# Kernel optimization log

Hardware: AMD Instinct MI355X
Metric: run time of the kernel (lower is better)

The kernel has to match this reference:

```python
import jax, jax.numpy as jnp
from jax import lax
import numpy as np

EPS = 1e-6
B, CIN, HW = 16, 12, 40
E, DEPTH, NH = 768, 12, 12
K, PAD = 10, 5
S = (HW + 2 * PAD - K) // 1 + 1  # 41 (series_len = s0); s1 also 41
L = S * S
HD = E // NH
MLP = 4 * E


def _ln(x, w, b):
    mu = x.mean(-1, keepdims=True)
    xc = x - mu
    var = (xc * xc).mean(-1, keepdims=True)
    return xc * lax.rsqrt(var + EPS) * w + b


def setup_inputs() -> dict:
    key = jax.random.key(0)
    ks = iter(jax.random.split(key, 24))
    r = lambda shape, s=0.02: jax.random.normal(next(ks), shape, jnp.float32) * s
    inp = {
        'x': jax.random.normal(next(ks), (B, CIN, HW, HW), jnp.float32),
        'conv_w': r((E, CIN, K, K)), 'conv_b': jnp.zeros((E,), jnp.float32),
        'pos_embed': r((1, L, E)),
        'ln1_w': jnp.ones((DEPTH, E), jnp.float32), 'ln1_b': jnp.zeros((DEPTH, E), jnp.float32),
        'qkv_w': r((DEPTH, E, 3 * E)), 'qkv_b': jnp.zeros((DEPTH, 3 * E), jnp.float32),
        'proj_w': r((DEPTH, E, E)), 'proj_b': jnp.zeros((DEPTH, E), jnp.float32),
        'ln2_w': jnp.ones((DEPTH, E), jnp.float32), 'ln2_b': jnp.zeros((DEPTH, E), jnp.float32),
        'fc1_w': r((DEPTH, E, MLP)), 'fc1_b': jnp.zeros((DEPTH, MLP), jnp.float32),
        'fc2_w': r((DEPTH, MLP, E)), 'fc2_b': jnp.zeros((DEPTH, E), jnp.float32),
        'lnf_w': jnp.ones((E,), jnp.float32), 'lnf_b': jnp.zeros((E,), jnp.float32),
        'tconv_w': r((E, 1, K, K)), 'tconv_b': jnp.zeros((1,), jnp.float32),
    }
    return inp


def reference(x, conv_w, conv_b, pos_embed, ln1_w, ln1_b, qkv_w, qkv_b,
              proj_w, proj_b, ln2_w, ln2_b, fc1_w, fc1_b, fc2_w, fc2_b,
              lnf_w, lnf_b, tconv_w, tconv_b):
    scale = HD ** -0.5
    # patch embed: Conv2d -> (B, E, 41, 41) -> flatten -> (B, L, E)
    h = lax.conv_general_dilated(x, conv_w, (1, 1), [(PAD, PAD), (PAD, PAD)])
    h = h + conv_b[None, :, None, None]
    t = h.reshape(B, E, L).transpose(0, 2, 1) + pos_embed

    for i in range(DEPTH):
        # attention over each of the S series slices (N = S tokens each), batched
        y = _ln(t, ln1_w[i], ln1_b[i])
        qkv = (y @ qkv_w[i] + qkv_b[i]).reshape(B, S, S, 3, NH, HD)
        q, k, v = qkv[:, :, :, 0], qkv[:, :, :, 1], qkv[:, :, :, 2]  # (B,S,N,NH,HD)
        attn = jnp.einsum('bsnhd,bsmhd->bshnm', q, k) * scale
        attn = jax.nn.softmax(attn, axis=-1)
        o = jnp.einsum('bshnm,bsmhd->bsnhd', attn, v).reshape(B, L, E)
        t = t + (o @ proj_w[i] + proj_b[i])
        # MLP
        z = _ln(t, ln2_w[i], ln2_b[i])
        z = jax.nn.gelu(z @ fc1_w[i] + fc1_b[i], approximate=False)
        t = t + (z @ fc2_w[i] + fc2_b[i])

    t = _ln(t, lnf_w, lnf_b)
    feat = t.reshape(B, S, S, E).transpose(0, 3, 1, 2)  # (B, E, 41, 41)
    # ConvTranspose2d(k=10, s=1, p=5) == direct conv with flipped/swapped kernel, pad k-1-p=4
    wt = jnp.flip(tconv_w, (2, 3)).transpose(1, 0, 2, 3)  # (out_c, E, K, K)
    out = lax.conv_general_dilated(feat, wt, (1, 1), [(K - 1 - PAD,) * 2] * 2)
    out = out + tconv_b[None, :, None, None]
    return jnp.squeeze(out)  # (B, 40, 40)
```

## Files before the change

### kernel.cpp

```cpp
#include <hip/hip_runtime.h>
#include <cstdint>

typedef __bf16 bf16_t;
typedef __attribute__((ext_vector_type(8))) __bf16 bf16x8;
typedef __attribute__((ext_vector_type(4))) __bf16 bf16x4;
typedef __attribute__((ext_vector_type(4))) float f32x4;

#define TOKENS 26896
#define LLEN   1681
#define SDIM   41
#define EDIM   768

__device__ __forceinline__ void gload_lds16(const bf16_t* g, bf16_t* l) {
  auto gp = reinterpret_cast<const __attribute__((address_space(1))) char*>(
      reinterpret_cast<uintptr_t>(g));
  auto lp = reinterpret_cast<__attribute__((address_space(3))) char*>(
      reinterpret_cast<uintptr_t>(l));
  __builtin_amdgcn_global_load_lds(gp, lp, 16, 0, 0);
}

enum { EPI_T_POS = 0, EPI_BF16 = 1, EPI_ADD_T = 2, EPI_GELU = 3, EPI_F32 = 4 };

template <int EPI>
__global__ __launch_bounds__(256, 4) void gemm4_kernel(
    const bf16_t* __restrict__ A, const bf16_t* __restrict__ Bt,
    const float* __restrict__ bias, float* __restrict__ fout,
    bf16_t* __restrict__ bout, const float* __restrict__ pos,
    int M, int N, int K, int ntn, int nwg)
{
  __shared__ bf16_t lds[16384];
  const int tid = threadIdx.x, wave = tid >> 6, lane = tid & 63;
  const int wr = wave >> 1, wc = wave & 1;

  int id = blockIdx.x;
  {
    const int q = nwg >> 3, r = nwg & 7;
    const int xcd = id & 7, ix = id >> 3;
    id = (xcd < r ? xcd * (q + 1) : r * (q + 1) + (xcd - r) * q) + ix;
  }
  const int row0 = (id / ntn) * 128;
  const int col0 = (id % ntn) * 128;
  const int NT = K >> 5;

  const int srow = tid >> 2;
  const int sswz = ((tid & 3) ^ ((srow >> 1) & 3)) * 8;
  const bf16_t* aptr[2];
  const bf16_t* bptr[2];
  #pragma unroll
  for (int p = 0; p < 2; ++p) {
    int ar = row0 + p * 64 + srow; if (ar > M - 1) ar = M - 1;
    int br = col0 + p * 64 + srow; if (br > N - 1) br = N - 1;
    aptr[p] = A  + (size_t)ar * K + sswz;
    bptr[p] = Bt + (size_t)br * K + sswz;
  }
  bf16_t* sdst = lds + tid * 8;

  #define STAGE(BUF, KT) do {                                   \
    const int koff_ = (KT) << 5;                                \
    gload_lds16(aptr[0] + koff_, sdst + (BUF)*8192);            \
    gload_lds16(aptr[1] + koff_, sdst + (BUF)*8192 + 2048);     \
    gload_lds16(bptr[0] + koff_, sdst + (BUF)*8192 + 4096);     \
    gload_lds16(bptr[1] + koff_, sdst + (BUF)*8192 + 6144);     \
  } while (0)

  const int l15 = lane & 15, l4 = lane >> 4;
  const int fswz = (l4 ^ ((l15 >> 1) & 3)) << 3;
  const bf16_t* lA = lds + (wr * 64 + l15) * 32 + fswz;
  const bf16_t* lB = lds + 4096 + (wc * 64 + l15) * 32 + fswz;

  f32x4 acc[4][4] = {};

  #define COMPUTE(BUF) do {                                     \
    bf16x8 fa[4], fb[4];                                        \
    _Pragma("unroll")                                           \
    for (int m_ = 0; m_ < 4; ++m_) fa[m_] = *(const bf16x8*)(lA + (BUF)*8192 + m_*512); \
    _Pragma("unroll")                                           \
    for (int n_ = 0; n_ < 4; ++n_) fb[n_] = *(const bf16x8*)(lB + (BUF)*8192 + n_*512); \
    _Pragma("unroll")                                           \
    for (int m_ = 0; m_ < 4; ++m_)                              \
      _Pragma("unroll")                                         \
      for (int n_ = 0; n_ < 4; ++n_)                            \
        acc[m_][n_] = __builtin_amdgcn_mfma_f32_16x16x32_bf16(fa[m_], fb[n_], acc[m_][n_], 0, 0, 0); \
  } while (0)

  STAGE(0, 0);
  __syncthreads();
  int kt = 0;
  while (kt + 2 <= NT) {
    if (kt + 1 < NT) STAGE(1, kt + 1);
    COMPUTE(0);
    __syncthreads();
    if (kt + 2 < NT) STAGE(0, kt + 2);
    COMPUTE(1);
    __syncthreads();
    kt += 2;
  }
  if (kt < NT) COMPUTE(0);
  #undef STAGE
  #undef COMPUTE

  const int rgrp = lane >> 4;
  #pragma unroll
  for (int m = 0; m < 4; ++m) {
    #pragma unroll
    for (int n = 0; n < 4; ++n) {
      const int col = col0 + wc * 64 + n * 16 + l15;
      if (col >= N) continue;
      const int rbase = row0 + wr * 64 + m * 16 + rgrp * 4;
      float bv = 0.f;
      if constexpr (EPI != EPI_F32) bv = bias[col];
      #pragma unroll
      for (int r = 0; r < 4; ++r) {
        const int rr = rbase + r;
        if (rr >= M) continue;
        const float v = acc[m][n][r] + bv;
        const size_t o = (size_t)rr * N + col;
        if constexpr (EPI == EPI_T_POS) {
          const int l = rr % LLEN;
          bout[o] = (bf16_t)(v + pos[(size_t)l * N + col]);
        } else if constexpr (EPI == EPI_BF16) {
          bout[o] = (bf16_t)v;
        } else if constexpr (EPI == EPI_ADD_T) {
          bout[o] = (bf16_t)((float)bout[o] + v);
        } else if constexpr (EPI == EPI_GELU) {
          const float gg = 0.5f * v * (1.f + erff(v * 0.70710678118654752f));
          bout[o] = (bf16_t)gg;
        } else {
          fout[o] = v;
        }
      }
    }
  }
}

__global__ __launch_bounds__(256) void gemm128_f32(
    const bf16_t* __restrict__ A, const bf16_t* __restrict__ Bt,
    float* __restrict__ fout, int M, int N, int K)
{
  __shared__ bf16_t As[128 * 32];
  __shared__ bf16_t Bs[128 * 32];
  const int tid = threadIdx.x, wave = tid >> 6, lane = tid & 63;
  const int row0 = blockIdx.x * 128, col0 = blockIdx.y * 128;
  const int wr = wave >> 1, wc = wave & 1;
  f32x4 acc[4][4] = {};
  const int srow = lane >> 2, skoff = (lane & 3) * 8;
  const int nsteps = K >> 5;
  for (int kt = 0; kt < nsteps; ++kt) {
    const int k0 = kt << 5;
    #pragma unroll
    for (int i = 0; i < 2; ++i) {
      const int r = (i * 4 + wave) * 16 + srow;
      int arow = row0 + r; if (arow > M - 1) arow = M - 1;
      int brow = col0 + r; if (brow > N - 1) brow = N - 1;
      gload_lds16(A  + (size_t)arow * K + k0 + skoff, &As[r * 32 + skoff]);
      gload_lds16(Bt + (size_t)brow * K + k0 + skoff, &Bs[r * 32 + skoff]);
    }
    asm volatile("s_waitcnt vmcnt(0)" ::: "memory");
    __syncthreads();
    const int lrow = lane & 15, lk = (lane >> 4) * 8;
    bf16x8 af[4], bfr[4];
    #pragma unroll
    for (int mi = 0; mi < 4; ++mi)
      af[mi] = *(const bf16x8*)&As[(wr * 64 + mi * 16 + lrow) * 32 + lk];
    #pragma unroll
    for (int ni = 0; ni < 4; ++ni)
      bfr[ni] = *(const bf16x8*)&Bs[(wc * 64 + ni * 16 + lrow) * 32 + lk];
    #pragma unroll
    for (int mi = 0; mi < 4; ++mi)
      #pragma unroll
      for (int ni = 0; ni < 4; ++ni)
        acc[mi][ni] = __builtin_amdgcn_mfma_f32_16x16x32_bf16(af[mi], bfr[ni], acc[mi][ni], 0, 0, 0);
    __syncthreads();
  }
  const int lcol = lane & 15, rgrp = lane >> 4;
  #pragma unroll
  for (int mi = 0; mi < 4; ++mi)
    #pragma unroll
    for (int ni = 0; ni < 4; ++ni) {
      const int col = col0 + wc * 64 + ni * 16 + lcol;
      if (col >= N) continue;
      const int rbase = row0 + wr * 64 + mi * 16 + rgrp * 4;
      #pragma unroll
      for (int r = 0; r < 4; ++r) {
        const int rr = rbase + r;
        if (rr >= M) continue;
        fout[(size_t)rr * N + col] = acc[mi][ni][r];
      }
    }
}

__global__ __launch_bounds__(256) void ln_kernel(
    const bf16_t* __restrict__ t, const float* __restrict__ w,
    const float* __restrict__ b, bf16_t* __restrict__ y)
{
  const int token = blockIdx.x * 4 + (threadIdx.x >> 6);
  const int lane  = threadIdx.x & 63;
  const bf16_t* xp = t + (size_t)token * EDIM;
  const bf16x8 a8 = *(const bf16x8*)(xp + lane * 8);
  const bf16x4 a4 = *(const bf16x4*)(xp + 512 + lane * 4);
  float va[12];
  #pragma unroll
  for (int j = 0; j < 8; ++j) va[j] = (float)a8[j];
  #pragma unroll
  for (int j = 0; j < 4; ++j) va[8 + j] = (float)a4[j];
  float s = 0.f;
  #pragma unroll
  for (int j = 0; j < 12; ++j) s += va[j];
  #pragma unroll
  for (int off = 32; off; off >>= 1) s += __shfl_xor(s, off);
  const float mu = s * (1.f / 768.f);
  float q = 0.f;
  #pragma unroll
  for (int j = 0; j < 12; ++j) { const float d = va[j] - mu; q += d * d; }
  #pragma unroll
  for (int off = 32; off; off >>= 1) q += __shfl_xor(q, off);
  const float rs = rsqrtf(q * (1.f / 768.f) + 1e-6f);

  bf16_t* yp = y + (size_t)token * EDIM;
  {
    const int e0 = lane * 8;
    const float4 w0 = ((const float4*)(w + e0))[0];
    const float4 w1 = ((const float4*)(w + e0))[1];
    const float4 b0 = ((const float4*)(b + e0))[0];
    const float4 b1 = ((const float4*)(b + e0))[1];
    bf16x8 o;
    o[0] = (bf16_t)((va[0] - mu) * rs * w0.x + b0.x);
    o[1] = (bf16_t)((va[1] - mu) * rs * w0.y + b0.y);
    o[2] = (bf16_t)((va[2] - mu) * rs * w0.z + b0.z);
    o[3] = (bf16_t)((va[3] - mu) * rs * w0.w + b0.w);
    o[4] = (bf16_t)((va[4] - mu) * rs * w1.x + b1.x);
    o[5] = (bf16_t)((va[5] - mu) * rs * w1.y + b1.y);
    o[6] = (bf16_t)((va[6] - mu) * rs * w1.z + b1.z);
    o[7] = (bf16_t)((va[7] - mu) * rs * w1.w + b1.w);
    *(bf16x8*)(yp + e0) = o;
  }
  {
    const int e0 = 512 + lane * 4;
    const float4 w0 = *(const float4*)(w + e0);
    const float4 b0 = *(const float4*)(b + e0);
    bf16x4 o;
    o[0] = (bf16_t)((va[8]  - mu) * rs * w0.x + b0.x);
    o[1] = (bf16_t)((va[9]  - mu) * rs * w0.y + b0.y);
    o[2] = (bf16_t)((va[10] - mu) * rs * w0.z + b0.z);
    o[3] = (bf16_t)((va[11] - mu) * rs * w0.w + b0.w);
    *(bf16x4*)(yp + e0) = o;
  }
}

__global__ __launch_bounds__(256) void attn_kernel(
    const bf16_t* __restrict__ qkv, bf16_t* __restrict__ o)
{
  const int blk = blockIdx.x;
  const int h  = blk % 12;
  const int bs = blk / 12;
  const int s1 = bs % SDIM;
  const int b  = bs / SDIM;
  __shared__ float Qs[SDIM][65], Ks[SDIM][65], Vs[SDIM][65], Ps[SDIM][44];
  const int tid = threadIdx.x;
  const size_t base = ((size_t)b * LLEN + (size_t)s1 * SDIM);

  for (int idx = tid; idx < SDIM * 8; idx += 256) {
    const int m = idx >> 3, c = idx & 7;
    const bf16_t* p = qkv + (base + m) * 2304 + h * 64 + c * 8;
    const bf16x8 qv = *(const bf16x8*)(p);
    const bf16x8 kv = *(const bf16x8*)(p + 768);
    const bf16x8 vv = *(const bf16x8*)(p + 1536);
    #pragma unroll
    for (int j = 0; j < 8; ++j) {
      Qs[m][c * 8 + j] = (float)qv[j];
      Ks[m][c * 8 + j] = (float)kv[j];
      Vs[m][c * 8 + j] = (float)vv[j];
    }
  }
  __syncthreads();

  for (int idx = tid; idx < SDIM * SDIM; idx += 256) {
    const int n = idx / SDIM, m = idx % SDIM;
    float s = 0.f;
    #pragma unroll
    for (int d = 0; d < 64; ++d) s += Qs[n][d] * Ks[m][d];
    Ps[n][m] = s * 0.125f;
  }
  __syncthreads();

  {
    const int row = tid >> 2, sub = tid & 3;
    if (row < SDIM) {
      float mx = -1e30f;
      for (int m = sub; m < SDIM; m += 4) mx = fmaxf(mx, Ps[row][m]);
      mx = fmaxf(mx, __shfl_xor(mx, 1));
      mx = fmaxf(mx, __shfl_xor(mx, 2));
      float sum = 0.f;
      for (int m = sub; m < SDIM; m += 4) {
        const float e = __expf(Ps[row][m] - mx);
        Ps[row][m] = e;
        sum += e;
      }
      sum += __shfl_xor(sum, 1);
      sum += __shfl_xor(sum, 2);
      const float inv = 1.f / sum;
      for (int m = sub; m < SDIM; m += 4) Ps[row][m] *= inv;
    }
  }
  __syncthreads();

  for (int idx = tid; idx < SDIM * 64; idx += 256) {
    const int n = idx >> 6, d = idx & 63;
    float s = 0.f;
    #pragma unroll
    for (int m = 0; m < SDIM; ++m) s += Ps[n][m] * Vs[m][d];
    o[(base + n) * EDIM + h * 64 + d] = (bf16_t)s;
  }
}

__global__ __launch_bounds__(256) void transpose_kernel(
    const float* __restrict__ in, bf16_t* __restrict__ out, int K, int N)
{
  __shared__ float tile[32][33];
  const int k0 = blockIdx.x * 32, n0 = blockIdx.y * 32;
  const int tx = threadIdx.x & 31, ty = threadIdx.x >> 5;
  #pragma unroll
  for (int i = 0; i < 32; i += 8) {
    const int k = k0 + ty + i, n = n0 + tx;
    if (k < K && n < N) tile[ty + i][tx] = in[(size_t)k * N + n];
  }
  __syncthreads();
  #pragma unroll
  for (int i = 0; i < 32; i += 8) {
    const int n = n0 + ty + i, k = k0 + tx;
    if (n < N && k < K) out[(size_t)n * K + k] = (bf16_t)tile[tx][ty + i];
  }
}

__global__ __launch_bounds__(256) void im2col_kernel(
    const float* __restrict__ x, bf16_t* __restrict__ col, int tok0, int ntok)
{
  const size_t idx = (size_t)blockIdx.x * 256 + threadIdx.x;
  if (idx >= (size_t)ntok * 1216) return;
  const int kk = (int)(idx % 1216);
  const size_t tok = tok0 + idx / 1216;
  const int b = (int)(tok / LLEN), l = (int)(tok % LLEN);
  const int s1 = l / SDIM, s2 = l % SDIM;
  float v = 0.f;
  if (kk < 1200) {
    const int cin = kk / 100, r = kk % 100, ky = r / 10, kx = r % 10;
    const int iy = s1 - 5 + ky, ix = s2 - 5 + kx;
    if (iy >= 0 && iy < 40 && ix >= 0 && ix < 40)
      v = x[((size_t)(b * 12 + cin) * 40 + iy) * 40 + ix];
  }
  col[idx] = (bf16_t)v;
}

__global__ __launch_bounds__(256) void convw_kernel(
    const float* __restrict__ w, bf16_t* __restrict__ out)
{
  const int idx = blockIdx.x * 256 + threadIdx.x;
  const int kk = idx % 1216, e = idx / 1216;
  const float v = (kk < 1200) ? w[(size_t)e * 1200 + kk] : 0.f;
  out[idx] = (bf16_t)v;
}

__global__ __launch_bounds__(256) void tconvw_kernel(
    const float* __restrict__ w, bf16_t* __restrict__ out)
{
  const int idx = blockIdx.x * 256 + threadIdx.x;
  const int e = idx % 768, tap = idx / 768;
  const int ky = tap / 10, kx = tap % 10;
  out[idx] = (bf16_t)w[(size_t)e * 100 + (9 - ky) * 10 + (9 - kx)];
}

__global__ __launch_bounds__(256) void outconv_kernel(
    const float* __restrict__ g, const float* __restrict__ tb,
    float* __restrict__ out)
{
  const int idx = blockIdx.x * 256 + threadIdx.x;
  if (idx >= 16 * 40 * 40) return;
  const int x = idx % 40, y = (idx / 40) % 40, b = idx / 1600;
  float s = tb[0];
  #pragma unroll
  for (int ky = 0; ky < 10; ++ky) {
    const int ty_ = y - 4 + ky;
    if (ty_ < 0 || ty_ >= SDIM) continue;
    #pragma unroll
    for (int kx = 0; kx < 10; ++kx) {
      const int tx_ = x - 4 + kx;
      if (tx_ < 0 || tx_ >= SDIM) continue;
      s += g[((size_t)b * LLEN + ty_ * SDIM + tx_) * 100 + ky * 10 + kx];
    }
  }
  out[idx] = s;
}

extern "C" void kernel_launch(void* const* d_in, const int* in_sizes, int n_in,
                              void* d_out, int out_size, void* d_ws, size_t ws_size,
                              hipStream_t stream)
{
  const float* x       = (const float*)d_in[0];
  const float* conv_w  = (const float*)d_in[1];
  const float* conv_b  = (const float*)d_in[2];
  const float* pos     = (const float*)d_in[3];
  const float* ln1_w   = (const float*)d_in[4];
  const float* ln1_b   = (const float*)d_in[5];
  const float* qkv_w   = (const float*)d_in[6];
  const float* qkv_b   = (const float*)d_in[7];
  const float* proj_w  = (const float*)d_in[8];
  const float* proj_b  = (const float*)d_in[9];
  const float* ln2_w   = (const float*)d_in[10];
  const float* ln2_b   = (const float*)d_in[11];
  const float* fc1_w   = (const float*)d_in[12];
  const float* fc1_b   = (const float*)d_in[13];
  const float* fc2_w   = (const float*)d_in[14];
  const float* fc2_b   = (const float*)d_in[15];
  const float* lnf_w   = (const float*)d_in[16];
  const float* lnf_b   = (const float*)d_in[17];
  const float* tconv_w = (const float*)d_in[18];
  const float* tconv_b = (const float*)d_in[19];
  float* out = (float*)d_out;

  const int nch = (ws_size >= 262200000UL) ? 1
                : (ws_size >= 179500000UL) ? 2 : 4;
  const int cht = TOKENS / nch;

  char* p = (char*)d_ws;
  auto alloc = [&](size_t bytes) {
    char* r = p;
    p += (bytes + 255) & ~(size_t)255;
    return r;
  };
  bf16_t* wbuf = (bf16_t*)alloc((size_t)768 * 9216 * 2);
  bf16_t* t    = (bf16_t*)alloc((size_t)TOKENS * EDIM * 2);
  bf16_t* ybuf = (bf16_t*)alloc((size_t)TOKENS * EDIM * 2);
  bf16_t* hbuf = (bf16_t*)alloc((size_t)cht * 3072 * 2);

  bf16_t* Wq = wbuf;
  bf16_t* Wp = Wq + (size_t)2304 * 768;
  bf16_t* W1 = Wp + (size_t)768 * 768;
  bf16_t* W2 = W1 + (size_t)3072 * 768;

  auto g4 = [&](int epi, const bf16_t* A, const bf16_t* Bt,
                const float* bias, bf16_t* bo, const float* pe,
                int M, int N, int K) {
    const int mtiles = (M + 127) / 128;
    const int ntn = N / 128;
    const int nwg = mtiles * ntn;
    switch (epi) {
      case EPI_T_POS: gemm4_kernel<EPI_T_POS><<<nwg, 256, 0, stream>>>(A, Bt, bias, nullptr, bo, pe, M, N, K, ntn, nwg); break;
      case EPI_BF16:  gemm4_kernel<EPI_BF16 ><<<nwg, 256, 0, stream>>>(A, Bt, bias, nullptr, bo, pe, M, N, K, ntn, nwg); break;
      case EPI_ADD_T: gemm4_kernel<EPI_ADD_T><<<nwg, 256, 0, stream>>>(A, Bt, bias, nullptr, bo, pe, M, N, K, ntn, nwg); break;
      default:        gemm4_kernel<EPI_GELU ><<<nwg, 256, 0, stream>>>(A, Bt, bias, nullptr, bo, pe, M, N, K, ntn, nwg); break;
    }
  };

  convw_kernel<<<(768 * 1216) / 256, 256, 0, stream>>>(conv_w, wbuf);
  for (int c = 0; c < nch; ++c) {
    const int tok0 = c * cht;
    im2col_kernel<<<(unsigned)(((size_t)cht * 1216 + 255) / 256), 256, 0, stream>>>(x, hbuf, tok0, cht);
    g4(EPI_T_POS, hbuf, wbuf, conv_b, t + (size_t)tok0 * EDIM, pos, cht, EDIM, 1216);
  }

  for (int i = 0; i < 12; ++i) {
    transpose_kernel<<<dim3(24, 72), 256, 0, stream>>>(qkv_w + (size_t)i * 768 * 2304, Wq, 768, 2304);
    transpose_kernel<<<dim3(24, 24), 256, 0, stream>>>(proj_w + (size_t)i * 768 * 768, Wp, 768, 768);
    transpose_kernel<<<dim3(24, 96), 256, 0, stream>>>(fc1_w + (size_t)i * 768 * 3072, W1, 768, 3072);
    transpose_kernel<<<dim3(96, 24), 256, 0, stream>>>(fc2_w + (size_t)i * 3072 * 768, W2, 3072, 768);

    ln_kernel<<<TOKENS / 4, 256, 0, stream>>>(t, ln1_w + i * EDIM, ln1_b + i * EDIM, ybuf);
    for (int c = 0; c < nch; ++c) {
      const size_t ro = (size_t)c * cht;
      g4(EPI_BF16, ybuf + ro * EDIM, Wq, qkv_b + i * 2304, hbuf, nullptr, cht, 2304, 768);
      attn_kernel<<<(16 / nch) * SDIM * 12, 256, 0, stream>>>(hbuf, ybuf + ro * EDIM);
    }
    g4(EPI_ADD_T, ybuf, Wp, proj_b + i * EDIM, t, nullptr, TOKENS, EDIM, 768);

    ln_kernel<<<TOKENS / 4, 256, 0, stream>>>(t, ln2_w + i * EDIM, ln2_b + i * EDIM, ybuf);
    for (int c = 0; c < nch; ++c) {
      const size_t ro = (size_t)c * cht;
      g4(EPI_GELU, ybuf + ro * EDIM, W1, fc1_b + i * 3072, hbuf, nullptr, cht, 3072, 768);
      g4(EPI_ADD_T, hbuf, W2, fc2_b + i * EDIM, t + ro * EDIM, nullptr, cht, EDIM, 3072);
    }
  }

  ln_kernel<<<TOKENS / 4, 256, 0, stream>>>(t, lnf_w, lnf_b, ybuf);
  tconvw_kernel<<<(100 * 768) / 256, 256, 0, stream>>>(tconv_w, wbuf);
  gemm128_f32<<<dim3((TOKENS + 127) / 128, 1), 256, 0, stream>>>(ybuf, wbuf, (float*)hbuf, TOKENS, 100, 768);
  outconv_kernel<<<100, 256, 0, stream>>>((const float*)hbuf, tconv_b, out);
}
```

Measured before the change: 10.20 ms.

## Triple-buffer GEMM LDS with vmcnt waits and use tanh-approx GELU

```diff
diff --git a/kernel.cpp b/kernel.cpp
--- a/kernel.cpp
+++ b/kernel.cpp
@@ -22,13 +22,13 @@
 enum { EPI_T_POS = 0, EPI_BF16 = 1, EPI_ADD_T = 2, EPI_GELU = 3, EPI_F32 = 4 };
 
 template <int EPI>
-__global__ __launch_bounds__(256, 4) void gemm4_kernel(
+__global__ __launch_bounds__(256, 3) void gemm4_kernel(
     const bf16_t* __restrict__ A, const bf16_t* __restrict__ Bt,
     const float* __restrict__ bias, float* __restrict__ fout,
     bf16_t* __restrict__ bout, const float* __restrict__ pos,
     int M, int N, int K, int ntn, int nwg)
 {
-  __shared__ bf16_t lds[16384];
+  __shared__ bf16_t lds[3 * 8192];
   const int tid = threadIdx.x, wave = tid >> 6, lane = tid & 63;
   const int wr = wave >> 1, wc = wave & 1;
 
@@ -83,19 +83,31 @@
         acc[m_][n_] = __builtin_amdgcn_mfma_f32_16x16x32_bf16(fa[m_], fb[n_], acc[m_][n_], 0, 0, 0); \
   } while (0)
 
+  #define STEP(SC, SN, T) do {                                  \
+    if ((T) + 2 < NT) STAGE(SN, (T) + 2);                       \
+    COMPUTE(SC);                                                \
+    if ((T) + 2 < NT)      asm volatile("s_waitcnt vmcnt(4)" ::: "memory"); \
+    else if ((T) + 1 < NT) asm volatile("s_waitcnt vmcnt(0)" ::: "memory"); \
+    __builtin_amdgcn_s_barrier();                               \
+    __builtin_amdgcn_sched_barrier(0);                          \
+  } while (0)
+
   STAGE(0, 0);
-  __syncthreads();
-  int kt = 0;
-  while (kt + 2 <= NT) {
-    if (kt + 1 < NT) STAGE(1, kt + 1);
-    COMPUTE(0);
-    __syncthreads();
-    if (kt + 2 < NT) STAGE(0, kt + 2);
-    COMPUTE(1);
-    __syncthreads();
-    kt += 2;
-  }
-  if (kt < NT) COMPUTE(0);
+  if (NT > 1) {
+    STAGE(1, 1);
+    asm volatile("s_waitcnt vmcnt(4)" ::: "memory");
+  } else {
+    asm volatile("s_waitcnt vmcnt(0)" ::: "memory");
+  }
+  __builtin_amdgcn_s_barrier();
+  __builtin_amdgcn_sched_barrier(0);
+
+  for (int kt = 0; kt < NT; kt += 3) {
+    STEP(0, 2, kt);
+    if (kt + 1 < NT) STEP(1, 0, kt + 1);
+    if (kt + 2 < NT) STEP(2, 1, kt + 2);
+  }
+  #undef STEP
   #undef STAGE
   #undef COMPUTE
 
@@ -123,7 +135,8 @@
         } else if constexpr (EPI == EPI_ADD_T) {
           bout[o] = (bf16_t)((float)bout[o] + v);
         } else if constexpr (EPI == EPI_GELU) {
-          const float gg = 0.5f * v * (1.f + erff(v * 0.70710678118654752f));
+          const float u = v + 0.044715f * v * v * v;
+          const float gg = v / (1.f + __expf(-1.5957691216f * u));
           bout[o] = (bf16_t)gg;
         } else {
           fout[o] = v;
```

Result: no change. 10.00 ms (-1.9%).
